# Performance work log

Hardware: AMD Instinct MI355X
Metric: run time of the kernel (lower is better)

The kernel has to match this reference:

```python
import jax, jax.numpy as jnp
import numpy as np

V, D, H, HID, L, C, R, ALPHA = 32000, 768, 12, 3072, 2, 2, 8, 16
B, S = 64, 512
HD = D // H
SCALE = ALPHA / R

def _lin(x, W, b, A, Bm):
    # LoRA linear (eval mode, dropout=identity): x @ W^T + b + scaling * (x @ A^T) @ B^T
    return x @ W.T + b + (x @ A.T) @ Bm.T * SCALE

def _ln(x, g, b):
    m = x.mean(-1, keepdims=True)
    v = ((x - m) ** 2).mean(-1, keepdims=True)
    return (x - m) / jnp.sqrt(v + 1e-5) * g + b

def setup_inputs():
    ks = iter(jax.random.split(jax.random.key(0), 64))
    def nrm(shape):
        return jax.random.normal(next(ks), shape, dtype=jnp.float32) * 0.02
    inp = {"tokens": jax.random.randint(next(ks), (B, S), 0, V)}
    inp["emb_W"] = nrm((V, D)); inp["emb_A"] = nrm((R, V)); inp["emb_B"] = nrm((D, R))
    dims = {"q": (D, D), "k": (D, D), "v": (D, D), "o": (D, D), "1": (D, HID), "2": (HID, D)}
    for nm, (di, do) in dims.items():
        inp["W" + nm] = nrm((L, do, di)); inp["b" + nm] = jnp.zeros((L, do), jnp.float32)
        inp["A" + nm] = nrm((L, R, di)); inp["B" + nm] = nrm((L, do, R))
    inp["g1"] = jnp.ones((L, D), jnp.float32); inp["be1"] = jnp.zeros((L, D), jnp.float32)
    inp["g2"] = jnp.ones((L, D), jnp.float32); inp["be2"] = jnp.zeros((L, D), jnp.float32)
    inp["fcW"] = nrm((C, D)); inp["fcb"] = jnp.zeros((C,), jnp.float32)
    inp["fcA"] = nrm((R, D)); inp["fcB"] = nrm((C, R))
    return inp

def reference(tokens, emb_W, emb_A, emb_B,
              Wq, bq, Aq, Bq, Wk, bk, Ak, Bk, Wv, bv, Av, Bv, Wo, bo, Ao, Bo,
              W1, b1, A1, B1, W2, b2, A2, B2,
              g1, be1, g2, be2, fcW, fcb, fcA, fcB):
    # LoRA embedding: W[tok] + scaling * A^T[tok] @ B^T
    x = emb_W[tokens] + (emb_A.T[tokens] @ emb_B.T) * SCALE      # (B, S, D)
    x = jnp.transpose(x, (1, 0, 2))                              # (S, B, D)
    for l in range(L):
        Q = _lin(x, Wq[l], bq[l], Aq[l], Bq[l]).reshape(S, B, H, HD).transpose(0, 2, 1, 3)
        K = _lin(x, Wk[l], bk[l], Ak[l], Bk[l]).reshape(S, B, H, HD).transpose(0, 2, 1, 3)
        Vt = _lin(x, Wv[l], bv[l], Av[l], Bv[l]).reshape(S, B, H, HD).transpose(0, 2, 1, 3)
        # Faithful to the source: attention mixes over the BATCH axis (S, H, B, B)
        scores = jnp.einsum('shbd,shcd->shbc', Q, K) / jnp.sqrt(jnp.float32(HD))
        probs = jax.nn.softmax(scores, axis=-1)
        ao = jnp.einsum('shbc,shcd->shbd', probs, Vt).transpose(0, 2, 1, 3).reshape(S, B, D)
        ao = _lin(ao, Wo[l], bo[l], Ao[l], Bo[l])
        x = _ln(x + ao, g1[l], be1[l])
        ff = _lin(jax.nn.relu(_lin(x, W1[l], b1[l], A1[l], B1[l])), W2[l], b2[l], A2[l], B2[l])
        x = _ln(x + ff, g2[l], be2[l])
    return _lin(x.mean(0), fcW, fcb, fcA, fcB)                   # (B, C)
```

## Files before the change

kernel.cpp:

```cpp
#include <hip/hip_runtime.h>
#include <hip/hip_bf16.h>

#define VSZ   32000
#define DSZ   768
#define HN    12
#define HIDSZ 3072
#define NL    2
#define CN    2
#define RR    8
#define SCALEF 2.0f
#define BBATCH 64
#define SSEQ  512
#define HDIM  64
#define NTOK  (BBATCH*SSEQ)
#define QKVM  (3*DSZ)

typedef __attribute__((ext_vector_type(8))) short bf16x8;
typedef __attribute__((ext_vector_type(4))) float floatx4;

__device__ __forceinline__ unsigned short f2bf_raw(float f) {
    __hip_bfloat16 h = __float2bfloat16(f);
    return __builtin_bit_cast(unsigned short, h);
}
__device__ __forceinline__ float bf2f(__hip_bfloat16 h) {
    return __bfloat162float(h);
}

__device__ __forceinline__ void gload16(const void* g, void* l) {
    __builtin_amdgcn_global_load_lds(
        (const __attribute__((address_space(1))) unsigned int*)g,
        (__attribute__((address_space(3))) unsigned int*)l, 16, 0, 0);
}

__global__ __launch_bounds__(256) void embed_kernel(
    const int* __restrict__ tokens, const float* __restrict__ embW,
    const float* __restrict__ embA, const float* __restrict__ embB,
    __hip_bfloat16* __restrict__ xb)
{
    int n = blockIdx.x;
    int s = n / BBATCH, b = n % BBATCH;
    int tok = tokens[b * SSEQ + s];
    __shared__ float a[RR];
    if (threadIdx.x < RR) a[threadIdx.x] = embA[(size_t)threadIdx.x * VSZ + tok];
    __syncthreads();
    for (int d = threadIdx.x; d < DSZ; d += 256) {
        float val = embW[(size_t)tok * DSZ + d];
        float lo = 0.f;
        #pragma unroll
        for (int r = 0; r < RR; ++r) lo += a[r] * embB[d * RR + r];
        xb[(size_t)n * DSZ + d] = __float2bfloat16(val + SCALEF * lo);
    }
}

__global__ __launch_bounds__(256) void weff_kernel(
    const float* __restrict__ W, const float* __restrict__ A,
    const float* __restrict__ Bm, __hip_bfloat16* __restrict__ Weff, int K)
{
    int i = blockIdx.x * 256 + threadIdx.x;
    int o = blockIdx.y;
    float acc = W[(size_t)o * K + i];
    #pragma unroll
    for (int r = 0; r < RR; ++r)
        acc += SCALEF * Bm[o * RR + r] * A[(size_t)r * K + i];
    Weff[(size_t)o * K + i] = __float2bfloat16(acc);
}

__global__ __launch_bounds__(256) void biascat_kernel(
    const float* __restrict__ b0, const float* __restrict__ b1v,
    const float* __restrict__ b2v, float* __restrict__ out)
{
    int t = blockIdx.y * 256 + threadIdx.x;
    const float* src = (blockIdx.x == 0) ? b0 : (blockIdx.x == 1) ? b1v : b2v;
    out[blockIdx.x * DSZ + t] = src[t];
}

#define BM2  256
#define BK2  64
#define ABUF (BM2*BK2)

#define SB0() __builtin_amdgcn_sched_barrier(0)

__device__ __forceinline__ void stage_half(
    const unsigned short* __restrict__ g, unsigned short* l,
    int h, int ld, int k0, int t, int sk)
{
    #pragma unroll
    for (int it = 0; it < 2; ++it) {
        int rl = it * 64 + (t >> 3);
        gload16(g + (size_t)(h * 128 + rl) * ld + k0 + sk,
                l + (size_t)(h * 1024 + it * 512 + t) * 8);
    }
}

template<bool RELU, bool ADDRES>
__device__ __forceinline__ void mgemm_body(
    const __hip_bfloat16* __restrict__ X, const __hip_bfloat16* __restrict__ W,
    const float* __restrict__ bias, const __hip_bfloat16* __restrict__ res,
    __hip_bfloat16* __restrict__ Y, int K, int ldx, int ldy)
{
    __shared__ __align__(16) unsigned short As[2 * ABUF];
    __shared__ __align__(16) unsigned short Bs[2 * ABUF];

    const int t    = threadIdx.x;
    const int wv   = t >> 6;
    const int lane = t & 63;
    const int fm   = lane & 15;
    const int fq   = lane >> 4;
    const int wm   = wv >> 2;
    const int wn   = wv & 3;

    const int nbx = gridDim.x;
    const int nby = gridDim.y;
    int lin = blockIdx.y * nbx + blockIdx.x;
    {
        const int nwg = nbx * nby;
        int q = nwg >> 3, r = nwg & 7;
        int xcd = lin & 7, idx = lin >> 3;
        lin = (xcd < r ? xcd * (q + 1) : r * (q + 1) + (xcd - r) * q) + idx;
    }
    const int bn = lin % nby;
    const int bm = lin / nby;

    const unsigned short* Xg = (const unsigned short*)X + (size_t)bm * 256 * ldx;
    const unsigned short* Wg = (const unsigned short*)W + (size_t)bn * 256 * K;
    const int sk = ((t & 7) ^ ((t >> 3) & 7)) * 8;
    const int nt = K / BK2;

    floatx4 acc[2][2][4][2];
    #pragma unroll
    for (int a = 0; a < 2; ++a)
        #pragma unroll
        for (int b = 0; b < 2; ++b)
            #pragma unroll
            for (int c = 0; c < 4; ++c)
                #pragma unroll
                for (int d = 0; d < 2; ++d)
                    acc[a][b][c][d] = (floatx4){0.f, 0.f, 0.f, 0.f};

    const int swzg = (fq ^ (fm & 7)) * 8;
    int aoff[4], boff[2];
    #pragma unroll
    for (int mf = 0; mf < 4; ++mf) aoff[mf] = (wm * 64 + mf * 16 + fm) * 64 + swzg;
    #pragma unroll
    for (int nf = 0; nf < 2; ++nf) boff[nf] = (wn * 32 + nf * 16 + fm) * 64 + swzg;

    stage_half(Xg, As, 0, ldx, 0, t, sk);
    stage_half(Wg, Bs, 0, K,   0, t, sk);
    stage_half(Xg, As, 1, ldx, 0, t, sk);
    stage_half(Wg, Bs, 1, K,   0, t, sk);
    if (nt > 1) {
        stage_half(Xg, As + ABUF, 0, ldx, BK2, t, sk);
        stage_half(Wg, Bs + ABUF, 0, K,   BK2, t, sk);
        stage_half(Wg, Bs + ABUF, 1, K,   BK2, t, sk);
        asm volatile("s_waitcnt vmcnt(6)" ::: "memory");
    } else {
        asm volatile("s_waitcnt vmcnt(0)" ::: "memory");
    }
    SB0();
    __builtin_amdgcn_s_barrier();
    SB0();

    for (int kt = 0; kt < nt; ++kt) {
        const unsigned short* Ab = As + (kt & 1) * ABUF;
        const unsigned short* Bb = Bs + (kt & 1) * ABUF;
        unsigned short* Aoth  = As + ((kt & 1) ^ 1) * ABUF;
        unsigned short* Asame = (unsigned short*)Ab;
        unsigned short* Bsame = (unsigned short*)Bb;
        const int k1 = (kt + 1) * BK2;
        const int k2 = (kt + 2) * BK2;
        bf16x8 af0[4][2], af1[4][2], bf0[2][2], bf1[2][2];

        #pragma unroll
        for (int mf = 0; mf < 4; ++mf) {
            af0[mf][0] = *(const bf16x8*)&Ab[aoff[mf]];
            af0[mf][1] = *(const bf16x8*)&Ab[aoff[mf] ^ 32];
        }
        #pragma unroll
        for (int nf = 0; nf < 2; ++nf) {
            bf0[nf][0] = *(const bf16x8*)&Bb[boff[nf]];
            bf0[nf][1] = *(const bf16x8*)&Bb[boff[nf] ^ 32];
        }
        SB0();
        if (kt + 1 < nt) stage_half(Xg, Aoth, 1, ldx, k1, t, sk);
        SB0();
        asm volatile("s_waitcnt lgkmcnt(0)" ::: "memory");
        SB0();
        __builtin_amdgcn_s_setprio(1);
        #pragma unroll
        for (int mf = 0; mf < 4; ++mf)
            #pragma unroll
            for (int nf = 0; nf < 2; ++nf) {
                acc[0][0][mf][nf] = __builtin_amdgcn_mfma_f32_16x16x32_bf16(
                    af0[mf][0], bf0[nf][0], acc[0][0][mf][nf], 0, 0, 0);
                acc[0][0][mf][nf] = __builtin_amdgcn_mfma_f32_16x16x32_bf16(
                    af0[mf][1], bf0[nf][1], acc[0][0][mf][nf], 0, 0, 0);
            }
        __builtin_amdgcn_s_setprio(0);
        SB0();
        __builtin_amdgcn_s_barrier();
        SB0();

        #pragma unroll
        for (int nf = 0; nf < 2; ++nf) {
            bf1[nf][0] = *(const bf16x8*)&Bb[(boff[nf] + 8192)];
            bf1[nf][1] = *(const bf16x8*)&Bb[(boff[nf] + 8192) ^ 32];
        }
        SB0();
        if (kt + 2 < nt) stage_half(Xg, Asame, 0, ldx, k2, t, sk);
        SB0();
        asm volatile("s_waitcnt lgkmcnt(0)" ::: "memory");
        SB0();
        __builtin_amdgcn_s_setprio(1);
        #pragma unroll
        for (int mf = 0; mf < 4; ++mf)
            #pragma unroll
            for (int nf = 0; nf < 2; ++nf) {
                acc[0][1][mf][nf] = __builtin_amdgcn_mfma_f32_16x16x32_bf16(
                    af0[mf][0], bf1[nf][0], acc[0][1][mf][nf], 0, 0, 0);
                acc[0][1][mf][nf] = __builtin_amdgcn_mfma_f32_16x16x32_bf16(
                    af0[mf][1], bf1[nf][1], acc[0][1][mf][nf], 0, 0, 0);
            }
        __builtin_amdgcn_s_setprio(0);
        SB0();
        __builtin_amdgcn_s_barrier();
        SB0();

        #pragma unroll
        for (int mf = 0; mf < 4; ++mf) {
            af1[mf][0] = *(const bf16x8*)&Ab[(aoff[mf] + 8192)];
            af1[mf][1] = *(const bf16x8*)&Ab[(aoff[mf] + 8192) ^ 32];
        }
        SB0();
        if (kt + 2 < nt) stage_half(Wg, Bsame, 0, K, k2, t, sk);
        SB0();
        asm volatile("s_waitcnt lgkmcnt(0)" ::: "memory");
        SB0();
        __builtin_amdgcn_s_setprio(1);
        #pragma unroll
        for (int mf = 0; mf < 4; ++mf)
            #pragma unroll
            for (int nf = 0; nf < 2; ++nf) {
                acc[1][0][mf][nf] = __builtin_amdgcn_mfma_f32_16x16x32_bf16(
                    af1[mf][0], bf0[nf][0], acc[1][0][mf][nf], 0, 0, 0);
                acc[1][0][mf][nf] = __builtin_amdgcn_mfma_f32_16x16x32_bf16(
                    af1[mf][1], bf0[nf][1], acc[1][0][mf][nf], 0, 0, 0);
            }
        __builtin_amdgcn_s_setprio(0);
        SB0();
        __builtin_amdgcn_s_barrier();
        SB0();

        if (kt + 2 < nt) stage_half(Wg, Bsame, 1, K, k2, t, sk);
        SB0();
        __builtin_amdgcn_s_setprio(1);
        #pragma unroll
        for (int mf = 0; mf < 4; ++mf)
            #pragma unroll
            for (int nf = 0; nf < 2; ++nf) {
                acc[1][1][mf][nf] = __builtin_amdgcn_mfma_f32_16x16x32_bf16(
                    af1[mf][0], bf1[nf][0], acc[1][1][mf][nf], 0, 0, 0);
                acc[1][1][mf][nf] = __builtin_amdgcn_mfma_f32_16x16x32_bf16(
                    af1[mf][1], bf1[nf][1], acc[1][1][mf][nf], 0, 0, 0);
            }
        __builtin_amdgcn_s_setprio(0);
        SB0();
        if (kt + 2 < nt) {
            asm volatile("s_waitcnt vmcnt(6)" ::: "memory");
        } else if (kt + 1 < nt) {
            asm volatile("s_waitcnt vmcnt(0)" ::: "memory");
        }
        SB0();
        __builtin_amdgcn_s_barrier();
        SB0();
    }

    #pragma unroll
    for (int mh = 0; mh < 2; ++mh)
        #pragma unroll
        for (int nh = 0; nh < 2; ++nh)
            #pragma unroll
            for (int nf = 0; nf < 2; ++nf) {
                const int col = bn * 256 + nh * 128 + wn * 32 + nf * 16 + fm;
                const float bj = bias[col];
                #pragma unroll
                for (int mf = 0; mf < 4; ++mf) {
                    const int row0 = bm * 256 + mh * 128 + wm * 64 + mf * 16 + fq * 4;
                    #pragma unroll
                    for (int r = 0; r < 4; ++r) {
                        float v = acc[mh][nh][mf][nf][r] + bj;
                        if (RELU) v = fmaxf(v, 0.f);
                        size_t off = (size_t)(row0 + r) * ldy + col;
                        if (ADDRES) v += bf2f(res[off]);
                        Y[off] = __float2bfloat16(v);
                    }
                }
            }
}

__global__ __launch_bounds__(512, 2) void gemm_qkv(
    const __hip_bfloat16* __restrict__ X, const __hip_bfloat16* __restrict__ W,
    const float* __restrict__ bias, const __hip_bfloat16* __restrict__ res,
    __hip_bfloat16* __restrict__ Y, int K, int ldx, int ldy)
{ mgemm_body<false, false>(X, W, bias, res, Y, K, ldx, ldy); }

__global__ __launch_bounds__(512, 2) void gemm_oproj(
    const __hip_bfloat16* __restrict__ X, const __hip_bfloat16* __restrict__ W,
    const float* __restrict__ bias, const __hip_bfloat16* __restrict__ res,
    __hip_bfloat16* __restrict__ Y, int K, int ldx, int ldy)
{ mgemm_body<false, true>(X, W, bias, res, Y, K, ldx, ldy); }

__global__ __launch_bounds__(512, 2) void gemm_ff1(
    const __hip_bfloat16* __restrict__ X, const __hip_bfloat16* __restrict__ W,
    const float* __restrict__ bias, const __hip_bfloat16* __restrict__ res,
    __hip_bfloat16* __restrict__ Y, int K, int ldx, int ldy)
{ mgemm_body<true, false>(X, W, bias, res, Y, K, ldx, ldy); }

__global__ __launch_bounds__(512, 2) void gemm_ff2(
    const __hip_bfloat16* __restrict__ X, const __hip_bfloat16* __restrict__ W,
    const float* __restrict__ bias, const __hip_bfloat16* __restrict__ res,
    __hip_bfloat16* __restrict__ Y, int K, int ldx, int ldy)
{ mgemm_body<false, true>(X, W, bias, res, Y, K, ldx, ldy); }

__global__ __launch_bounds__(256) void attn_kernel(
    const __hip_bfloat16* __restrict__ qkvb, __hip_bfloat16* __restrict__ aob)
{
    __shared__ __align__(16) unsigned short Vt[64][72];
    __shared__ __align__(16) unsigned short Ps[4][16][72];
    const int t    = threadIdx.x;
    const int wv   = t >> 6;
    const int lane = t & 63;
    const int fm   = lane & 15;
    const int fq   = lane >> 4;
    const int sp   = blockIdx.x / HN;
    const int h    = blockIdx.x % HN;
    const unsigned short* qg =
        (const unsigned short*)qkvb + (size_t)sp * BBATCH * QKVM + h * HDIM;

    {
        const int c = lane, d0 = wv * 16;
        const unsigned short* vrow = qg + 2 * DSZ + (size_t)c * QKVM + d0;
        bf16x8 v0 = *(const bf16x8*)vrow;
        bf16x8 v1 = *(const bf16x8*)(vrow + 8);
        #pragma unroll
        for (int i = 0; i < 8; ++i) {
            Vt[d0 + i][c]     = (unsigned short)v0[i];
            Vt[d0 + 8 + i][c] = (unsigned short)v1[i];
        }
    }

    const unsigned short* qrow = qg + (size_t)(wv * 16 + fm) * QKVM + fq * 8;
    bf16x8 af0 = *(const bf16x8*)qrow;
    bf16x8 af1 = *(const bf16x8*)(qrow + 32);
    bf16x8 bk0[4], bk1[4];
    #pragma unroll
    for (int jt = 0; jt < 4; ++jt) {
        const unsigned short* krow = qg + DSZ + (size_t)(jt * 16 + fm) * QKVM + fq * 8;
        bk0[jt] = *(const bf16x8*)krow;
        bk1[jt] = *(const bf16x8*)(krow + 32);
    }

    floatx4 sc[4];
    #pragma unroll
    for (int jt = 0; jt < 4; ++jt) sc[jt] = (floatx4){0.f, 0.f, 0.f, 0.f};
    #pragma unroll
    for (int jt = 0; jt < 4; ++jt) {
        sc[jt] = __builtin_amdgcn_mfma_f32_16x16x32_bf16(af0, bk0[jt], sc[jt], 0, 0, 0);
        sc[jt] = __builtin_amdgcn_mfma_f32_16x16x32_bf16(af1, bk1[jt], sc[jt], 0, 0, 0);
    }
    #pragma unroll
    for (int jt = 0; jt < 4; ++jt)
        #pragma unroll
        for (int r = 0; r < 4; ++r) sc[jt][r] *= 0.125f;

    float pr[4][4];
    #pragma unroll
    for (int r = 0; r < 4; ++r) {
        float m = fmaxf(fmaxf(sc[0][r], sc[1][r]), fmaxf(sc[2][r], sc[3][r]));
        #pragma unroll
        for (int msk = 1; msk < 16; msk <<= 1) m = fmaxf(m, __shfl_xor(m, msk, 64));
        float s = 0.f;
        #pragma unroll
        for (int jt = 0; jt < 4; ++jt) { pr[jt][r] = __expf(sc[jt][r] - m); s += pr[jt][r]; }
        #pragma unroll
        for (int msk = 1; msk < 16; msk <<= 1) s += __shfl_xor(s, msk, 64);
        float inv = 1.f / s;
        #pragma unroll
        for (int jt = 0; jt < 4; ++jt) pr[jt][r] *= inv;
    }

    #pragma unroll
    for (int jt = 0; jt < 4; ++jt)
        #pragma unroll
        for (int r = 0; r < 4; ++r)
            Ps[wv][fq * 4 + r][jt * 16 + fm] = f2bf_raw(pr[jt][r]);

    __syncthreads();

    bf16x8 ap0 = *(const bf16x8*)&Ps[wv][fm][fq * 8];
    bf16x8 ap1 = *(const bf16x8*)&Ps[wv][fm][32 + fq * 8];
    floatx4 ov[4];
    #pragma unroll
    for (int jt = 0; jt < 4; ++jt) ov[jt] = (floatx4){0.f, 0.f, 0.f, 0.f};
    #pragma unroll
    for (int jt = 0; jt < 4; ++jt) {
        bf16x8 bv0 = *(const bf16x8*)&Vt[jt * 16 + fm][fq * 8];
        bf16x8 bv1 = *(const bf16x8*)&Vt[jt * 16 + fm][32 + fq * 8];
        ov[jt] = __builtin_amdgcn_mfma_f32_16x16x32_bf16(ap0, bv0, ov[jt], 0, 0, 0);
        ov[jt] = __builtin_amdgcn_mfma_f32_16x16x32_bf16(ap1, bv1, ov[jt], 0, 0, 0);
    }

    __hip_bfloat16* obase = aob + ((size_t)sp * BBATCH + wv * 16 + fq * 4) * DSZ + h * HDIM;
    #pragma unroll
    for (int jt = 0; jt < 4; ++jt)
        #pragma unroll
        for (int r = 0; r < 4; ++r)
            obase[(size_t)r * DSZ + jt * 16 + fm] = __float2bfloat16(ov[jt][r]);
}

__device__ __forceinline__ float block_sum256(float vsum, volatile float* red) {
    #pragma unroll
    for (int off = 32; off > 0; off >>= 1) vsum += __shfl_down(vsum, off, 64);
    if ((threadIdx.x & 63) == 0) red[threadIdx.x >> 6] = vsum;
    __syncthreads();
    return red[0] + red[1] + red[2] + red[3];
}

__global__ __launch_bounds__(256) void ln_kernel(
    const __hip_bfloat16* __restrict__ src, __hip_bfloat16* __restrict__ dst,
    const float* __restrict__ g, const float* __restrict__ be)
{
    __shared__ float red1[4];
    __shared__ float red2[4];
    const int n = blockIdx.x;
    const int t = threadIdx.x;
    const __hip_bfloat16* row = src + (size_t)n * DSZ;
    __hip_bfloat16* orow = dst + (size_t)n * DSZ;
    float v0 = bf2f(row[t]), v1 = bf2f(row[t + 256]), v2 = bf2f(row[t + 512]);
    float total = block_sum256(v0 + v1 + v2, red1);
    float mean = total * (1.0f / DSZ);
    float d0 = v0 - mean, d1 = v1 - mean, d2 = v2 - mean;
    __syncthreads();
    float var = block_sum256(d0 * d0 + d1 * d1 + d2 * d2, red2) * (1.0f / DSZ);
    float rstd = rsqrtf(var + 1e-5f);
    orow[t]       = __float2bfloat16(d0 * rstd * g[t]       + be[t]);
    orow[t + 256] = __float2bfloat16(d1 * rstd * g[t + 256] + be[t + 256]);
    orow[t + 512] = __float2bfloat16(d2 * rstd * g[t + 512] + be[t + 512]);
}

__global__ __launch_bounds__(256) void meanS_kernel(
    const __hip_bfloat16* __restrict__ x, float* __restrict__ xm)
{
    int idx = blockIdx.x * 256 + threadIdx.x;
    int b = idx / DSZ, d = idx % DSZ;
    float acc = 0.f;
    for (int s = 0; s < SSEQ; ++s)
        acc += bf2f(x[((size_t)s * BBATCH + b) * DSZ + d]);
    xm[idx] = acc * (1.0f / SSEQ);
}

__global__ __launch_bounds__(128) void fc_kernel(
    const float* __restrict__ xm, const float* __restrict__ fcW,
    const float* __restrict__ fcb, const float* __restrict__ fcA,
    const float* __restrict__ fcBm, float* __restrict__ out)
{
    int t = threadIdx.x;
    if (t >= BBATCH * CN) return;
    int b = t / CN, c = t % CN;
    float acc = fcb[c];
    float lora[RR];
    #pragma unroll
    for (int r = 0; r < RR; ++r) lora[r] = 0.f;
    for (int d = 0; d < DSZ; ++d) {
        float xv = xm[b * DSZ + d];
        acc += xv * fcW[c * DSZ + d];
        #pragma unroll
        for (int r = 0; r < RR; ++r) lora[r] += xv * fcA[r * DSZ + d];
    }
    float lo = 0.f;
    #pragma unroll
    for (int r = 0; r < RR; ++r) lo += lora[r] * fcBm[c * RR + r];
    out[b * CN + c] = acc + SCALEF * lo;
}

extern "C" void kernel_launch(void* const* d_in, const int* in_sizes, int n_in,
                              void* d_out, int out_size, void* d_ws, size_t ws_size,
                              hipStream_t stream) {
    const int*   tokens = (const int*)  d_in[0];
    const float* embW   = (const float*)d_in[1];
    const float* embA   = (const float*)d_in[2];
    const float* embB   = (const float*)d_in[3];
    const float* Wq = (const float*)d_in[4],  *bq = (const float*)d_in[5],
               * Aq = (const float*)d_in[6],  *Bq = (const float*)d_in[7];
    const float* Wk = (const float*)d_in[8],  *bk = (const float*)d_in[9],
               * Ak = (const float*)d_in[10], *Bk = (const float*)d_in[11];
    const float* Wv = (const float*)d_in[12], *bv = (const float*)d_in[13],
               * Av = (const float*)d_in[14], *Bv = (const float*)d_in[15];
    const float* Wo = (const float*)d_in[16], *bo = (const float*)d_in[17],
               * Ao = (const float*)d_in[18], *Bo = (const float*)d_in[19];
    const float* W1 = (const float*)d_in[20], *b1 = (const float*)d_in[21],
               * A1 = (const float*)d_in[22], *B1 = (const float*)d_in[23];
    const float* W2 = (const float*)d_in[24], *b2 = (const float*)d_in[25],
               * A2 = (const float*)d_in[26], *B2 = (const float*)d_in[27];
    const float* g1 = (const float*)d_in[28], *be1 = (const float*)d_in[29];
    const float* g2 = (const float*)d_in[30], *be2 = (const float*)d_in[31];
    const float* fcW = (const float*)d_in[32], *fcb = (const float*)d_in[33];
    const float* fcA = (const float*)d_in[34], *fcBm = (const float*)d_in[35];

    const size_t ND = (size_t)NTOK * DSZ;

    const size_t X_F    = ND / 2;
    const size_t XT_F   = ND / 2;
    const size_t WQKV_F = (size_t)QKVM * DSZ / 2;
    const size_t WO_F   = (size_t)DSZ * DSZ / 2;
    const size_t WF1_F  = (size_t)HIDSZ * DSZ / 2;
    const size_t WF2_F  = (size_t)DSZ * HIDSZ / 2;
    const size_t BQKV_F = 2304;
    const size_t XM_F   = (size_t)BBATCH * DSZ;
    const size_t fixedF = X_F + XT_F + WQKV_F + WO_F + WF1_F + WF2_F + BQKV_F + XM_F;
    const size_t availF = ws_size / 4;

    int schunk = 2;
    const int cand[6] = {512, 256, 128, 64, 32, 16};
    for (int i = 0; i < 6; ++i) {
        size_t chunkF = (size_t)cand[i] * BBATCH * (HIDSZ / 2);
        if (fixedF + chunkF <= availF) { schunk = cand[i]; break; }
    }
    const int Nc = schunk * BBATCH;
    const int nchunk = SSEQ / schunk;

    float* p = (float*)d_ws;
    __hip_bfloat16* x  = (__hip_bfloat16*)p;     p += X_F;
    __hip_bfloat16* xt = (__hip_bfloat16*)p;     p += XT_F;
    __hip_bfloat16* wqkvb = (__hip_bfloat16*)p;  p += WQKV_F;
    __hip_bfloat16* wob   = (__hip_bfloat16*)p;  p += WO_F;
    __hip_bfloat16* wf1b  = (__hip_bfloat16*)p;  p += WF1_F;
    __hip_bfloat16* wf2b  = (__hip_bfloat16*)p;  p += WF2_F;
    float* bqkv = p;                             p += BQKV_F;
    float* xm   = p;                             p += XM_F;
    __hip_bfloat16* cb16 = (__hip_bfloat16*)p;
    __hip_bfloat16* qkvb = cb16;
    __hip_bfloat16* aob  = cb16 + (size_t)Nc * QKVM;
    __hip_bfloat16* hb   = cb16;

    embed_kernel<<<NTOK, 256, 0, stream>>>(tokens, embW, embA, embB, x);

    for (int l = 0; l < NL; ++l) {
        const size_t oDD = (size_t)l * DSZ * DSZ;
        const size_t oDH = (size_t)l * HIDSZ * DSZ;
        const size_t oRD = (size_t)l * RR * DSZ;
        const size_t oRH = (size_t)l * RR * HIDSZ;
        const size_t oDR = (size_t)l * DSZ * RR;
        const size_t oHR = (size_t)l * HIDSZ * RR;

        weff_kernel<<<dim3(3, DSZ), 256, 0, stream>>>(Wq + oDD, Aq + oRD, Bq + oDR, wqkvb, DSZ);
        weff_kernel<<<dim3(3, DSZ), 256, 0, stream>>>(Wk + oDD, Ak + oRD, Bk + oDR, wqkvb + (size_t)DSZ * DSZ, DSZ);
        weff_kernel<<<dim3(3, DSZ), 256, 0, stream>>>(Wv + oDD, Av + oRD, Bv + oDR, wqkvb + (size_t)2 * DSZ * DSZ, DSZ);
        biascat_kernel<<<dim3(3, 3), 256, 0, stream>>>(bq + (size_t)l * DSZ, bk + (size_t)l * DSZ, bv + (size_t)l * DSZ, bqkv);
        weff_kernel<<<dim3(3, DSZ), 256, 0, stream>>>(Wo + oDD, Ao + oRD, Bo + oDR, wob, DSZ);
        weff_kernel<<<dim3(3, HIDSZ), 256, 0, stream>>>(W1 + oDH, A1 + oRD, B1 + oHR, wf1b, DSZ);
        weff_kernel<<<dim3(12, DSZ), 256, 0, stream>>>(W2 + oDH, A2 + oRH, B2 + oDR, wf2b, HIDSZ);

        const float* bo_l = bo + (size_t)l * DSZ;
        const float* b1_l = b1 + (size_t)l * HIDSZ;
        const float* b2_l = b2 + (size_t)l * DSZ;

        for (int c = 0; c < nchunk; ++c) {
            __hip_bfloat16* xc  = x  + (size_t)c * Nc * DSZ;
            __hip_bfloat16* xtc = xt + (size_t)c * Nc * DSZ;

            gemm_qkv<<<dim3(Nc / BM2, QKVM / BM2), 512, 0, stream>>>(
                xc, wqkvb, bqkv, nullptr, qkvb, DSZ, DSZ, QKVM);

            attn_kernel<<<schunk * HN, 256, 0, stream>>>(qkvb, aob);

            gemm_oproj<<<dim3(Nc / BM2, DSZ / BM2), 512, 0, stream>>>(
                aob, wob, bo_l, xc, xtc, DSZ, DSZ, DSZ);
            ln_kernel<<<Nc, 256, 0, stream>>>(xtc, xc, g1 + (size_t)l * DSZ, be1 + (size_t)l * DSZ);

            const int nsub = (Nc >= 2 * BM2 && (Nc / 2) % BM2 == 0) ? 2 : 1;
            const int Mh = Nc / nsub;
            for (int sub = 0; sub < nsub; ++sub) {
                const size_t soff = (size_t)sub * Mh * DSZ;
                gemm_ff1<<<dim3(Mh / BM2, HIDSZ / BM2), 512, 0, stream>>>(
                    xc + soff, wf1b, b1_l, nullptr, hb, DSZ, DSZ, HIDSZ);
                gemm_ff2<<<dim3(Mh / BM2, DSZ / BM2), 512, 0, stream>>>(
                    hb, wf2b, b2_l, xc + soff, xtc + soff, HIDSZ, HIDSZ, DSZ);
            }
            ln_kernel<<<Nc, 256, 0, stream>>>(xtc, xc, g2 + (size_t)l * DSZ, be2 + (size_t)l * DSZ);
        }
    }

    meanS_kernel<<<(BBATCH * DSZ) / 256, 256, 0, stream>>>(x, xm);
    fc_kernel<<<1, 128, 0, stream>>>(xm, fcW, fcb, fcA, fcBm, (float*)d_out);
}
```

Baseline: 1.740 ms.

## Hoist all LDS fragment reads per k-tile and drop intermediate barriers in GEMM

The GEMM main loop now issues every A and B fragment read for a k-tile up front as inline-asm ds_read_b128 with immediate offsets. Partial lgkmcnt waits let each MFMA quadrant start once its operands have arrived. Two of the four per-iteration barriers are removed, and the next-next-tile global-to-LDS staging for the current buffer is moved to after the third quadrant's barrier. This cuts barrier stalls and LDS latency exposure, at the cost of more live registers and hand-counted waitcnt values that must match the compiler's instruction ordering.

After: 1.735 ms. Within noise of the previous version (-0.3%).

```diff
diff --git a/kernel.cpp b/kernel.cpp
--- a/kernel.cpp
+++ b/kernel.cpp
@@ -32,6 +32,13 @@
         (__attribute__((address_space(3))) unsigned int*)l, 16, 0, 0);
 }
 
+__device__ __forceinline__ bf16x8 dsr128(unsigned addr, int off) {
+    bf16x8 r;
+    asm volatile("ds_read_b128 %0, %1 offset:%2"
+                 : "=v"(r) : "v"(addr), "i"(off) : "memory");
+    return r;
+}
+
 __global__ __launch_bounds__(256) void embed_kernel(
     const int* __restrict__ tokens, const float* __restrict__ embW,
     const float* __restrict__ embA, const float* __restrict__ embB,
@@ -137,12 +144,12 @@
                 for (int d = 0; d < 2; ++d)
                     acc[a][b][c][d] = (floatx4){0.f, 0.f, 0.f, 0.f};
 
+    typedef __attribute__((address_space(3))) const unsigned short lds_cus;
+    const unsigned asb = (unsigned)(unsigned long long)(lds_cus*)As;
+    const unsigned bsb = (unsigned)(unsigned long long)(lds_cus*)Bs;
     const int swzg = (fq ^ (fm & 7)) * 8;
-    int aoff[4], boff[2];
-    #pragma unroll
-    for (int mf = 0; mf < 4; ++mf) aoff[mf] = (wm * 64 + mf * 16 + fm) * 64 + swzg;
-    #pragma unroll
-    for (int nf = 0; nf < 2; ++nf) boff[nf] = (wn * 32 + nf * 16 + fm) * 64 + swzg;
+    const unsigned aA0 = asb + (unsigned)(((wm * 64 + fm) * 64 + swzg) * 2);
+    const unsigned bB0 = bsb + (unsigned)(((wn * 32 + fm) * 64 + swzg) * 2);
 
     stage_half(Xg, As, 0, ldx, 0, t, sk);
     stage_half(Wg, Bs, 0, K,   0, t, sk);
@@ -161,29 +168,42 @@
     SB0();
 
     for (int kt = 0; kt < nt; ++kt) {
-        const unsigned short* Ab = As + (kt & 1) * ABUF;
-        const unsigned short* Bb = Bs + (kt & 1) * ABUF;
+        const unsigned aBk0 = aA0 + ((kt & 1) << 15);
+        const unsigned bBk0 = bB0 + ((kt & 1) << 15);
+        const unsigned aBk1 = aBk0 ^ 64u;
+        const unsigned bBk1 = bBk0 ^ 64u;
         unsigned short* Aoth  = As + ((kt & 1) ^ 1) * ABUF;
-        unsigned short* Asame = (unsigned short*)Ab;
-        unsigned short* Bsame = (unsigned short*)Bb;
+        unsigned short* Asame = As + (kt & 1) * ABUF;
+        unsigned short* Bsame = Bs + (kt & 1) * ABUF;
         const int k1 = (kt + 1) * BK2;
         const int k2 = (kt + 2) * BK2;
-        bf16x8 af0[4][2], af1[4][2], bf0[2][2], bf1[2][2];
+        bf16x8 af0[4][2], af1[4][2], b0f[2][2], b1f[2][2];
 
         #pragma unroll
         for (int mf = 0; mf < 4; ++mf) {
-            af0[mf][0] = *(const bf16x8*)&Ab[aoff[mf]];
-            af0[mf][1] = *(const bf16x8*)&Ab[aoff[mf] ^ 32];
+            af0[mf][0] = dsr128(aBk0, mf * 2048);
+            af0[mf][1] = dsr128(aBk1, mf * 2048);
         }
         #pragma unroll
         for (int nf = 0; nf < 2; ++nf) {
-            bf0[nf][0] = *(const bf16x8*)&Bb[boff[nf]];
-            bf0[nf][1] = *(const bf16x8*)&Bb[boff[nf] ^ 32];
+            b0f[nf][0] = dsr128(bBk0, nf * 2048);
+            b0f[nf][1] = dsr128(bBk1, nf * 2048);
+        }
+        #pragma unroll
+        for (int nf = 0; nf < 2; ++nf) {
+            b1f[nf][0] = dsr128(bBk0, 16384 + nf * 2048);
+            b1f[nf][1] = dsr128(bBk1, 16384 + nf * 2048);
+        }
+        #pragma unroll
+        for (int mf = 0; mf < 4; ++mf) {
+            af1[mf][0] = dsr128(aBk0, 16384 + mf * 2048);
+            af1[mf][1] = dsr128(aBk1, 16384 + mf * 2048);
         }
         SB0();
         if (kt + 1 < nt) stage_half(Xg, Aoth, 1, ldx, k1, t, sk);
         SB0();
-        asm volatile("s_waitcnt lgkmcnt(0)" ::: "memory");
+
+        asm volatile("s_waitcnt lgkmcnt(12)" ::: "memory");
         SB0();
         __builtin_amdgcn_s_setprio(1);
         #pragma unroll
@@ -191,24 +211,14 @@
             #pragma unroll
             for (int nf = 0; nf < 2; ++nf) {
                 acc[0][0][mf][nf] = __builtin_amdgcn_mfma_f32_16x16x32_bf16(
-                    af0[mf][0], bf0[nf][0], acc[0][0][mf][nf], 0, 0, 0);
+                    af0[mf][0], b0f[nf][0], acc[0][0][mf][nf], 0, 0, 0);
                 acc[0][0][mf][nf] = __builtin_amdgcn_mfma_f32_16x16x32_bf16(
-                    af0[mf][1], bf0[nf][1], acc[0][0][mf][nf], 0, 0, 0);
+                    af0[mf][1], b0f[nf][1], acc[0][0][mf][nf], 0, 0, 0);
             }
         __builtin_amdgcn_s_setprio(0);
         SB0();
-        __builtin_amdgcn_s_barrier();
-        SB0();
-
-        #pragma unroll
-        for (int nf = 0; nf < 2; ++nf) {
-            bf1[nf][0] = *(const bf16x8*)&Bb[(boff[nf] + 8192)];
-            bf1[nf][1] = *(const bf16x8*)&Bb[(boff[nf] + 8192) ^ 32];
-        }
-        SB0();
-        if (kt + 2 < nt) stage_half(Xg, Asame, 0, ldx, k2, t, sk);
-        SB0();
-        asm volatile("s_waitcnt lgkmcnt(0)" ::: "memory");
+
+        asm volatile("s_waitcnt lgkmcnt(8)" ::: "memory");
         SB0();
         __builtin_amdgcn_s_setprio(1);
         #pragma unroll
@@ -216,23 +226,13 @@
             #pragma unroll
             for (int nf = 0; nf < 2; ++nf) {
                 acc[0][1][mf][nf] = __builtin_amdgcn_mfma_f32_16x16x32_bf16(
-                    af0[mf][0], bf1[nf][0], acc[0][1][mf][nf], 0, 0, 0);
+                    af0[mf][0], b1f[nf][0], acc[0][1][mf][nf], 0, 0, 0);
                 acc[0][1][mf][nf] = __builtin_amdgcn_mfma_f32_16x16x32_bf16(
-                    af0[mf][1], bf1[nf][1], acc[0][1][mf][nf], 0, 0, 0);
+                    af0[mf][1], b1f[nf][1], acc[0][1][mf][nf], 0, 0, 0);
             }
         __builtin_amdgcn_s_setprio(0);
         SB0();
-        __builtin_amdgcn_s_barrier();
-        SB0();
-
-        #pragma unroll
-        for (int mf = 0; mf < 4; ++mf) {
-            af1[mf][0] = *(const bf16x8*)&Ab[(aoff[mf] + 8192)];
-            af1[mf][1] = *(const bf16x8*)&Ab[(aoff[mf] + 8192) ^ 32];
-        }
-        SB0();
-        if (kt + 2 < nt) stage_half(Wg, Bsame, 0, K, k2, t, sk);
-        SB0();
+
         asm volatile("s_waitcnt lgkmcnt(0)" ::: "memory");
         SB0();
         __builtin_amdgcn_s_setprio(1);
@@ -241,16 +241,20 @@
             #pragma unroll
             for (int nf = 0; nf < 2; ++nf) {
                 acc[1][0][mf][nf] = __builtin_amdgcn_mfma_f32_16x16x32_bf16(
-                    af1[mf][0], bf0[nf][0], acc[1][0][mf][nf], 0, 0, 0);
+                    af1[mf][0], b0f[nf][0], acc[1][0][mf][nf], 0, 0, 0);
                 acc[1][0][mf][nf] = __builtin_amdgcn_mfma_f32_16x16x32_bf16(
-                    af1[mf][1], bf0[nf][1], acc[1][0][mf][nf], 0, 0, 0);
+                    af1[mf][1], b0f[nf][1], acc[1][0][mf][nf], 0, 0, 0);
             }
         __builtin_amdgcn_s_setprio(0);
         SB0();
         __builtin_amdgcn_s_barrier();
         SB0();
 
-        if (kt + 2 < nt) stage_half(Wg, Bsame, 1, K, k2, t, sk);
+        if (kt + 2 < nt) {
+            stage_half(Xg, Asame, 0, ldx, k2, t, sk);
+            stage_half(Wg, Bsame, 0, K,   k2, t, sk);
+            stage_half(Wg, Bsame, 1, K,   k2, t, sk);
+        }
         SB0();
         __builtin_amdgcn_s_setprio(1);
         #pragma unroll
@@ -258,9 +262,9 @@
             #pragma unroll
             for (int nf = 0; nf < 2; ++nf) {
                 acc[1][1][mf][nf] = __builtin_amdgcn_mfma_f32_16x16x32_bf16(
-                    af1[mf][0], bf1[nf][0], acc[1][1][mf][nf], 0, 0, 0);
+                    af1[mf][0], b1f[nf][0], acc[1][1][mf][nf], 0, 0, 0);
                 acc[1][1][mf][nf] = __builtin_amdgcn_mfma_f32_16x16x32_bf16(
-                    af1[mf][1], bf1[nf][1], acc[1][1][mf][nf], 0, 0, 0);
+                    af1[mf][1], b1f[nf][1], acc[1][1][mf][nf], 0, 0, 0);
             }
         __builtin_amdgcn_s_setprio(0);
         SB0();
```
